# Kernel optimization log

Measured on AMD Instinct MI355X. Metric: run time of the kernel, lower is better.

The kernel has to match this reference:

```python
import jax, jax.numpy as jnp
import numpy as np
import math

N, H, E, G = 20000, 256, 320000, 1000
NF, NS = 64, 3           # sinusoid frequencies, spatial dims
DIS = 2 * NF * NS        # 384
EIN = 2 * H + 9 + DIS    # edge MLP input dim = 905


def silu(x):
    return x * jax.nn.sigmoid(x)


def sin_emb(x):
    # x: [E, 3] -> [E, 2*NF*3]
    freqs = 2.0 * math.pi * jnp.arange(NF, dtype=x.dtype)
    emb = (x[..., None] * freqs).reshape(x.shape[0], NF * NS)
    return jnp.concatenate([jnp.sin(emb), jnp.cos(emb)], axis=-1)


def layer_norm(x, gamma, beta, eps=1e-5):
    mu = jnp.mean(x, axis=-1, keepdims=True)
    var = jnp.var(x, axis=-1, keepdims=True)
    return (x - mu) * jax.lax.rsqrt(var + eps) * gamma + beta


def setup_inputs() -> dict:
    key = jax.random.key(0)
    ks = jax.random.split(key, 16)
    s = 0.02
    return {
        "node_features": jax.random.normal(ks[0], (N, H), jnp.float32),
        "lattices": jax.random.normal(ks[1], (G, 3, 3), jnp.float32),
        "edge_index": jax.random.randint(ks[2], (2, E), 0, N, dtype=jnp.int64),
        "edge2graph": jnp.sort(jax.random.randint(ks[3], (E,), 0, G, dtype=jnp.int64)),
        "frac_diff": jax.random.uniform(ks[4], (E, NS), jnp.float32),
        "num_atoms": jax.random.randint(ks[5], (G,), 0, 100, dtype=jnp.int64),
        "ln_gamma": jnp.ones((H,), jnp.float32),
        "ln_beta": jnp.zeros((H,), jnp.float32),
        "We1": jax.random.normal(ks[6], (EIN, H), jnp.float32) * s,
        "be1": jnp.zeros((H,), jnp.float32),
        "We2": jax.random.normal(ks[7], (H, H), jnp.float32) * s,
        "be2": jnp.zeros((H,), jnp.float32),
        "Wn1": jax.random.normal(ks[8], (2 * H, H), jnp.float32) * s,
        "bn1": jnp.zeros((H,), jnp.float32),
        "Wn2": jax.random.normal(ks[9], (H, H), jnp.float32) * s,
        "bn2": jnp.zeros((H,), jnp.float32),
    }


def reference(node_features, lattices, edge_index, edge2graph, frac_diff, num_atoms,
              ln_gamma, ln_beta, We1, be1, We2, be2, Wn1, bn1, Wn2, bn2):
    n = node_features.shape[0]
    h = layer_norm(node_features, ln_gamma, ln_beta)

    # edge model: gather + concat + MLP
    hi = h[edge_index[0]]                      # [E, H]
    hj = h[edge_index[1]]                      # [E, H]
    fd = sin_emb(frac_diff)                    # [E, DIS]
    ltl = jnp.einsum('gij,gkj->gik', lattices, lattices).reshape(-1, 9)  # non_symmetric: L @ L^T
    le = ltl[edge2graph]                       # [E, 9]
    x = jnp.concatenate([hi, hj, le, fd], axis=1)        # [E, EIN]
    e = silu(x @ We1 + be1)
    e = silu(e @ We2 + be2)                    # [E, H]

    # node model: scatter-mean + concat + MLP
    src = edge_index[0]
    sums = jax.ops.segment_sum(e, src, num_segments=n)   # [N, H]
    cnt = jax.ops.segment_sum(jnp.ones((e.shape[0],), e.dtype), src, num_segments=n)
    agg = sums / jnp.maximum(cnt, 1.0)[:, None]
    y = jnp.concatenate([h, agg], axis=1)                # [N, 2H]
    y = silu(y @ Wn1 + bn1)
    y = silu(y @ Wn2 + bn2)

    return node_features + y
```

## Files before the change

kernel.cpp:

```cpp
#include <hip/hip_runtime.h>

typedef unsigned short UST;
typedef __bf16 bf16x8 __attribute__((ext_vector_type(8)));
typedef float floatx4 __attribute__((ext_vector_type(4)));
typedef unsigned short ushort8v __attribute__((ext_vector_type(8)));
typedef unsigned short ushort4v __attribute__((ext_vector_type(4)));

#define N_NODES 20000
#define E_EDGES 320000
#define KE 928
#define M_PAD 20096

static __device__ __forceinline__ UST f2bf(float x){
  unsigned int u = __float_as_uint(x);
  u += 0x7fffu + ((u >> 16) & 1u);
  return (UST)(u >> 16);
}
static __device__ __forceinline__ float bf2f(UST u){
  return __uint_as_float(((unsigned int)u) << 16);
}
static __device__ __forceinline__ float siluf(float v){
  return v / (1.0f + __expf(-v));
}
static __device__ __forceinline__ void gll16(const void* g, void* lds){
  __builtin_amdgcn_global_load_lds(
      (const __attribute__((address_space(1))) unsigned int*)g,
      (__attribute__((address_space(3))) unsigned int*)lds, 16, 0, 0);
}

static __device__ __forceinline__ void mfma_step(const UST* As, const UST* Bs,
    floatx4 (&acc)[4][4], int lm, int quad, int wM, int wN){
  bf16x8 a[4], b[4];
#pragma unroll
  for (int i = 0; i < 4; ++i)
    a[i] = *(const bf16x8*)(As + (wM + i*16 + lm)*32 + quad*8);
#pragma unroll
  for (int i = 0; i < 4; ++i)
    b[i] = *(const bf16x8*)(Bs + (wN + i*16 + lm)*32 + quad*8);
#pragma unroll
  for (int mi = 0; mi < 4; ++mi)
#pragma unroll
    for (int ni = 0; ni < 4; ++ni)
      acc[mi][ni] = __builtin_amdgcn_mfma_f32_16x16x32_bf16(a[mi], b[ni], acc[mi][ni], 0, 0, 0);
}

static __device__ __forceinline__ void mfma_stage2(const UST* At, const UST* Bg,
    int Kb, floatx4 (&acc)[4][4], int lm, int quad, int wM, int wN){
#pragma unroll 2
  for (int k0 = 0; k0 < 256; k0 += 32){
    bf16x8 a[4], b[4];
#pragma unroll
    for (int i = 0; i < 4; ++i)
      a[i] = *(const bf16x8*)(At + (wM + i*16 + lm)*264 + k0 + quad*8);
#pragma unroll
    for (int i = 0; i < 4; ++i)
      b[i] = *(const bf16x8*)(Bg + (size_t)(wN + i*16 + lm)*Kb + k0 + quad*8);
#pragma unroll
    for (int mi = 0; mi < 4; ++mi)
#pragma unroll
      for (int ni = 0; ni < 4; ++ni)
        acc[mi][ni] = __builtin_amdgcn_mfma_f32_16x16x32_bf16(a[mi], b[ni], acc[mi][ni], 0, 0, 0);
  }
}

__global__ __launch_bounds__(256) void prep_all(
    const float* __restrict__ We1, const float* __restrict__ We2,
    const float* __restrict__ Wn1, const float* __restrict__ Wn2,
    const float* __restrict__ x, const float* __restrict__ gamma,
    const float* __restrict__ beta, const float* __restrict__ lat,
    const int* __restrict__ esrc, int* __restrict__ cnti,
    UST* __restrict__ W1T, UST* __restrict__ W2T,
    UST* __restrict__ Wn1T, UST* __restrict__ Wn2T,
    UST* __restrict__ h, float* __restrict__ ltl){
  int bid = blockIdx.x, t = threadIdx.x;
  if (bid < 928){
    int i = bid*256 + t;
    int n = i / KE, k = i % KE;
    float v = 0.0f;
    if (k < 512)      v = We1[(size_t)k*256 + n];
    else if (k < 896){
      int idx = k - 512, j = idx >> 1, b = idx & 1;
      v = We1[(size_t)(521 + b*192 + j)*256 + n];
    }
    else if (k < 905) v = We1[(size_t)(k-384)*256 + n];
    W1T[i] = f2bf(v);
  } else if (bid < 1184){
    int i = (bid-928)*256 + t;
    int n = i >> 8, k = i & 255;
    W2T[i]  = f2bf(We2[(size_t)k*256 + n]);
    Wn2T[i] = f2bf(Wn2[(size_t)k*256 + n]);
  } else if (bid < 1696){
    int i = (bid-1184)*256 + t;
    int n = i >> 9, k = i & 511;
    Wn1T[i] = f2bf(Wn1[(size_t)k*256 + n]);
  } else if (bid < 6696){
    int wave = t >> 6, lane = t & 63;
    int row = (bid-1696)*4 + wave;
    const float4* xp = (const float4*)(x + (size_t)row * 256);
    float4 v = xp[lane];
    float s  = v.x + v.y + v.z + v.w;
    float sq = v.x*v.x + v.y*v.y + v.z*v.z + v.w*v.w;
#pragma unroll
    for (int o = 32; o > 0; o >>= 1){ s += __shfl_xor(s, o); sq += __shfl_xor(sq, o); }
    float mu  = s * (1.0f/256.0f);
    float var = sq * (1.0f/256.0f) - mu*mu;
    float rs  = rsqrtf(var + 1e-5f);
    float4 g = ((const float4*)gamma)[lane];
    float4 b = ((const float4*)beta)[lane];
    ushort4v o4;
    o4[0] = f2bf((v.x-mu)*rs*g.x + b.x);
    o4[1] = f2bf((v.y-mu)*rs*g.y + b.y);
    o4[2] = f2bf((v.z-mu)*rs*g.z + b.z);
    o4[3] = f2bf((v.w-mu)*rs*g.w + b.w);
    *(ushort4v*)(h + (size_t)row*256 + lane*4) = o4;
  } else if (bid < 6732){
    int i = (bid-6696)*256 + t;
    if (i < 9000){
      int g = i / 9, ij = i % 9, a = ij / 3, b = ij % 3;
      const float* L = lat + g*9;
      ltl[i] = L[a*3+0]*L[b*3+0] + L[a*3+1]*L[b*3+1] + L[a*3+2]*L[b*3+2];
    }
  } else {
    int e = (bid-6732)*256 + t;
    if (e < E_EDGES) atomicAdd(&cnti[esrc[e]], 1);
  }
}

__global__ __launch_bounds__(256) void scan_kernel(const int* __restrict__ cnti,
    int* __restrict__ off, int* __restrict__ head){
  __shared__ int ps[256];
  int t = threadIdx.x;
  const int CH = 80;
  const int4* cp = (const int4*)cnti;
  int base = t * CH;
  int s = 0;
#pragma unroll 1
  for (int i = 0; i < CH/4; ++i){
    int4 v = cp[t*(CH/4) + i];
    int idx = base + i*4;
    if (idx   < N_NODES) s += v.x;
    if (idx+1 < N_NODES) s += v.y;
    if (idx+2 < N_NODES) s += v.z;
    if (idx+3 < N_NODES) s += v.w;
  }
  ps[t] = s; __syncthreads();
#pragma unroll 1
  for (int o = 1; o < 256; o <<= 1){
    int v = (t >= o) ? ps[t - o] : 0;
    __syncthreads();
    ps[t] += v;
    __syncthreads();
  }
  int run = (t > 0) ? ps[t-1] : 0;
#pragma unroll 1
  for (int i = 0; i < CH/4; ++i){
    int4 v = cp[t*(CH/4) + i];
    int idx = base + i*4;
    int a4[4] = {v.x, v.y, v.z, v.w};
#pragma unroll
    for (int j = 0; j < 4; ++j){
      int id = idx + j;
      if (id < N_NODES){ off[id] = run; head[id] = run; run += a4[j]; }
    }
  }
  if (t == 255) off[N_NODES] = run;
}

__global__ __launch_bounds__(256) void fill_kernel(const int* __restrict__ src,
    int* __restrict__ head, int* __restrict__ eidx, int* __restrict__ srcs){
  int e = blockIdx.x*256 + threadIdx.x;
  if (e < E_EDGES){
    int s = src[e];
    int p = atomicAdd(&head[s], 1);
    eidx[p] = e;
    srcs[p] = s;
  }
}

__global__ __launch_bounds__(512, 4)
void gemm_edge_fused(const UST* __restrict__ h, const int* __restrict__ ei,
                     const int* __restrict__ e2g, const float* __restrict__ fdif,
                     const float* __restrict__ ltl, const UST* __restrict__ W1T,
                     const float* __restrict__ be1, const int* __restrict__ eidx,
                     const UST* __restrict__ W2T, const float* __restrict__ be2,
                     const int* __restrict__ rownode, float* __restrict__ sums){
  __shared__ __attribute__((aligned(16))) UST lds[128*264];
  __shared__ int rn[128];
  UST* As0 = lds;
  UST* As1 = lds + 4096;
  UST* Bs0 = lds + 8192;
  UST* Bs1 = lds + 16384;
  UST* e1t = lds;
  UST* EsT = lds;
  int t = threadIdx.x;
  int bM = blockIdx.x;
  int rA = t >> 2, cA = (t & 3) * 8;
  int p0 = bM*128 + rA;
  int e0 = eidx[p0];
  int src0 = ei[e0];
  int dst0 = ei[E_EDGES + e0];
  int g0 = e2g[e0];
  float f0x = fdif[e0*3+0], f0y = fdif[e0*3+1], f0z = fdif[e0*3+2];
  size_t btb0 = (size_t)rA*KE + cA;
  size_t btb1 = btb0 + (size_t)128*KE;
  int lane = t & 63, lm = lane & 15, quad = lane >> 4;
  int wave = t >> 6, wM = (wave >> 2)*64, wN = (wave & 3)*64;
  floatx4 acc[4][4] = {};
  UST* a0d = &As0[rA*32 + cA];
  UST* a1d = &As1[rA*32 + cA];
  UST* b0d0 = &Bs0[rA*32 + cA];
  UST* b0d1 = &Bs0[(128+rA)*32 + cA];
  UST* b1d0 = &Bs1[rA*32 + cA];
  UST* b1d1 = &Bs1[(128+rA)*32 + cA];
  if (t < 128) rn[t] = rownode[bM*128 + t];

#pragma unroll 1
  for (int w = 0; w < 8; ++w){
    int k0 = w*64;
    const UST* srow = (w < 4) ? (h + (size_t)src0*256 + k0)
                              : (h + (size_t)dst0*256 + (k0 - 256));
    gll16(srow + cA,      a0d);
    gll16(srow + 32 + cA, a1d);
    gll16(W1T + btb0 + k0,      b0d0);
    gll16(W1T + btb1 + k0,      b0d1);
    gll16(W1T + btb0 + k0 + 32, b1d0);
    gll16(W1T + btb1 + k0 + 32, b1d1);
    __syncthreads();
    mfma_step(As0, Bs0, acc, lm, quad, wM, wN);
    mfma_step(As1, Bs1, acc, lm, quad, wM, wN);
    __syncthreads();
  }
#pragma unroll 1
  for (int w = 8; w < 14; ++w){
    int k0 = w*64;
    gll16(W1T + btb0 + k0,      b0d0);
    gll16(W1T + btb1 + k0,      b0d1);
    gll16(W1T + btb0 + k0 + 32, b1d0);
    gll16(W1T + btb1 + k0 + 32, b1d1);
    int jb0 = (k0 + cA - 512) >> 1;
    ushort8v o0, o1;
#pragma unroll
    for (int ii = 0; ii < 4; ++ii){
      int jj = jb0 + ii;
      int dim = jj >> 6; float kf = (float)(jj & 63);
      float fr = (dim == 0) ? f0x : ((dim == 1) ? f0y : f0z);
      float q = __builtin_amdgcn_fractf(fr * kf);
      o0[2*ii]   = f2bf(__builtin_amdgcn_sinf(q));
      o0[2*ii+1] = f2bf(__builtin_amdgcn_cosf(q));
    }
#pragma unroll
    for (int ii = 0; ii < 4; ++ii){
      int jj = jb0 + 16 + ii;
      int dim = jj >> 6; float kf = (float)(jj & 63);
      float fr = (dim == 0) ? f0x : ((dim == 1) ? f0y : f0z);
      float q = __builtin_amdgcn_fractf(fr * kf);
      o1[2*ii]   = f2bf(__builtin_amdgcn_sinf(q));
      o1[2*ii+1] = f2bf(__builtin_amdgcn_cosf(q));
    }
    *(ushort8v*)a0d = o0;
    *(ushort8v*)a1d = o1;
    __syncthreads();
    mfma_step(As0, Bs0, acc, lm, quad, wM, wN);
    mfma_step(As1, Bs1, acc, lm, quad, wM, wN);
    __syncthreads();
  }
  {
    gll16(W1T + btb0 + 896, b0d0);
    gll16(W1T + btb1 + 896, b0d1);
    ushort8v o0;
#pragma unroll
    for (int i = 0; i < 8; ++i){
      int c = cA + i;
      o0[i] = (c < 9) ? f2bf(ltl[g0*9 + c]) : (UST)0;
    }
    *(ushort8v*)a0d = o0;
    __syncthreads();
    mfma_step(As0, Bs0, acc, lm, quad, wM, wN);
  }
  __syncthreads();
#pragma unroll
  for (int mi = 0; mi < 4; ++mi)
#pragma unroll
    for (int r = 0; r < 4; ++r){
      int ml = wM + mi*16 + quad*4 + r;
#pragma unroll
      for (int ni = 0; ni < 4; ++ni){
        int nl = wN + ni*16 + lm;
        float v = acc[mi][ni][r] + be1[nl];
        e1t[ml*264 + nl] = f2bf(siluf(v));
      }
    }
  __syncthreads();

  floatx4 acc2[4][4] = {};
  mfma_stage2(e1t, W2T, 256, acc2, lm, quad, wM, wN);
  __syncthreads();

#pragma unroll
  for (int mi = 0; mi < 4; ++mi)
#pragma unroll
    for (int ni = 0; ni < 4; ++ni){
      int nl = wN + ni*16 + lm;
      int ml = wM + mi*16 + quad*4;
      ushort4v pk;
#pragma unroll
      for (int r = 0; r < 4; ++r)
        pk[r] = f2bf(siluf(acc2[mi][ni][r] + be2[nl]));
      *(ushort4v*)&EsT[nl*132 + ml] = pk;
    }
  __syncthreads();
  {
    int c = t & 255, hh = t >> 8;
    int rbeg = hh * 64;
    int cur = rn[rbeg];
    float run = 0.0f;
#pragma unroll 1
    for (int r = rbeg; r < rbeg + 64; r += 4){
      ushort4v v4 = *(const ushort4v*)&EsT[c*132 + r];
#pragma unroll
      for (int q2 = 0; q2 < 4; ++q2){
        int nd = rn[r + q2];
        if (nd != cur){ atomicAdd(&sums[(size_t)cur*256 + c], run); run = 0.0f; cur = nd; }
        run += bf2f(v4[q2]);
      }
    }
    atomicAdd(&sums[(size_t)cur*256 + c], run);
  }
}

__global__ __launch_bounds__(512, 4)
void gemm_node12(const UST* __restrict__ h, const float* __restrict__ sums,
                 const int* __restrict__ offs, const UST* __restrict__ B1,
                 const float* __restrict__ bn1, const UST* __restrict__ B2,
                 const float* __restrict__ bn2,
                 float* __restrict__ out_f, const float* __restrict__ resid){
  __shared__ __attribute__((aligned(16))) UST lds[128*264];
  UST* As0 = lds;
  UST* As1 = lds + 4096;
  UST* Bs0 = lds + 8192;
  UST* Bs1 = lds + 16384;
  UST* y1t = lds;
  int t = threadIdx.x;
  int bM = blockIdx.x;
  int rA = t >> 2, cA = (t & 3) * 8;
  int row = bM*128 + rA;
  bool valid = row < N_NODES;
  float inv = 0.0f;
  if (valid){
    int deg = offs[row+1] - offs[row];
    inv = 1.0f / fmaxf((float)deg, 1.0f);
  }
  const UST* hrow = h + (size_t)row*256;
  const float* srow = sums + (size_t)row*256;
  size_t bb0 = (size_t)rA*512 + cA;
  size_t bb1 = bb0 + (size_t)128*512;
  int lane = t & 63, lm = lane & 15, quad = lane >> 4;
  int wave = t >> 6, wM = (wave >> 2)*64, wN = (wave & 3)*64;
  floatx4 acc[4][4] = {};
  UST* a0d = &As0[rA*32 + cA];
  UST* a1d = &As1[rA*32 + cA];
  UST* b0d0 = &Bs0[rA*32 + cA];
  UST* b0d1 = &Bs0[(128+rA)*32 + cA];
  UST* b1d0 = &Bs1[rA*32 + cA];
  UST* b1d1 = &Bs1[(128+rA)*32 + cA];
  const ushort8v z8 = {0,0,0,0,0,0,0,0};
#pragma unroll 1
  for (int w = 0; w < 8; ++w){
    int k0 = w*64;
    if (k0 < 256){
      if (valid){
        gll16(hrow + k0 + cA,      a0d);
        gll16(hrow + k0 + 32 + cA, a1d);
      } else {
        *(ushort8v*)a0d = z8;
        *(ushort8v*)a1d = z8;
      }
    } else {
      ushort8v o0 = z8, o1 = z8;
      if (valid){
        int q = k0 - 256 + cA;
        float4 s0 = *(const float4*)(srow + q);
        float4 s1 = *(const float4*)(srow + q + 4);
        o0[0]=f2bf(s0.x*inv); o0[1]=f2bf(s0.y*inv); o0[2]=f2bf(s0.z*inv); o0[3]=f2bf(s0.w*inv);
        o0[4]=f2bf(s1.x*inv); o0[5]=f2bf(s1.y*inv); o0[6]=f2bf(s1.z*inv); o0[7]=f2bf(s1.w*inv);
        float4 s2 = *(const float4*)(srow + q + 32);
        float4 s3 = *(const float4*)(srow + q + 36);
        o1[0]=f2bf(s2.x*inv); o1[1]=f2bf(s2.y*inv); o1[2]=f2bf(s2.z*inv); o1[3]=f2bf(s2.w*inv);
        o1[4]=f2bf(s3.x*inv); o1[5]=f2bf(s3.y*inv); o1[6]=f2bf(s3.z*inv); o1[7]=f2bf(s3.w*inv);
      }
      *(ushort8v*)a0d = o0;
      *(ushort8v*)a1d = o1;
    }
    gll16(B1 + bb0 + k0,      b0d0);
    gll16(B1 + bb1 + k0,      b0d1);
    gll16(B1 + bb0 + k0 + 32, b1d0);
    gll16(B1 + bb1 + k0 + 32, b1d1);
    __syncthreads();
    mfma_step(As0, Bs0, acc, lm, quad, wM, wN);
    mfma_step(As1, Bs1, acc, lm, quad, wM, wN);
    __syncthreads();
  }
  __syncthreads();
#pragma unroll
  for (int mi = 0; mi < 4; ++mi)
#pragma unroll
    for (int r = 0; r < 4; ++r){
      int ml = wM + mi*16 + quad*4 + r;
#pragma unroll
      for (int ni = 0; ni < 4; ++ni){
        int nl = wN + ni*16 + lm;
        y1t[ml*264 + nl] = f2bf(siluf(acc[mi][ni][r] + bn1[nl]));
      }
    }
  __syncthreads();
  floatx4 acc2[4][4] = {};
  mfma_stage2(y1t, B2, 256, acc2, lm, quad, wM, wN);
  int mbase = bM*128 + wM + quad*4;
  int nbase = wN + lm;
#pragma unroll
  for (int mi = 0; mi < 4; ++mi)
#pragma unroll
    for (int r = 0; r < 4; ++r){
      int m = mbase + mi*16 + r;
      if (m < N_NODES){
#pragma unroll
        for (int ni = 0; ni < 4; ++ni){
          int n = nbase + ni*16;
          float v = siluf(acc2[mi][ni][r] + bn2[n]);
          out_f[(size_t)m*256 + n] = resid[(size_t)m*256 + n] + v;
        }
      }
    }
}

extern "C" void kernel_launch(void* const* d_in, const int* in_sizes, int n_in,
                              void* d_out, int out_size, void* d_ws, size_t ws_size,
                              hipStream_t stream){
  (void)in_sizes; (void)n_in; (void)out_size; (void)ws_size;
  const float* node_features = (const float*)d_in[0];
  const float* lattices      = (const float*)d_in[1];
  const int*   edge_index    = (const int*)d_in[2];
  const int*   edge2graph    = (const int*)d_in[3];
  const float* frac_diff     = (const float*)d_in[4];
  const float* ln_gamma      = (const float*)d_in[6];
  const float* ln_beta       = (const float*)d_in[7];
  const float* We1 = (const float*)d_in[8];
  const float* be1 = (const float*)d_in[9];
  const float* We2 = (const float*)d_in[10];
  const float* be2 = (const float*)d_in[11];
  const float* Wn1 = (const float*)d_in[12];
  const float* bn1 = (const float*)d_in[13];
  const float* Wn2 = (const float*)d_in[14];
  const float* bn2 = (const float*)d_in[15];

  char* w = (char*)d_ws;
  size_t off_b = 0;
  auto carve = [&](size_t bytes) -> char* {
    char* p = w + off_b; off_b += (bytes + 1023) & ~(size_t)1023; return p;
  };
  UST*   W1T  = (UST*)carve((size_t)256*KE*2);
  UST*   W2T  = (UST*)carve((size_t)256*256*2);
  UST*   Wn1T = (UST*)carve((size_t)256*512*2);
  UST*   Wn2T = (UST*)carve((size_t)256*256*2);
  UST*   hbf  = (UST*)carve((size_t)N_NODES*256*2);
  float* ltl  = (float*)carve((size_t)9000*4);
  int*   cnti = (int*)carve((size_t)20480*4);
  int*   offs = (int*)carve((size_t)(N_NODES+1)*4);
  int*   head = (int*)carve((size_t)N_NODES*4);
  int*   eidx = (int*)carve((size_t)E_EDGES*4);
  int*   srcs = (int*)carve((size_t)E_EDGES*4);
  float* sums = (float*)carve((size_t)N_NODES*256*4);

  hipMemsetAsync(cnti, 0, (size_t)20480*4, stream);
  hipMemsetAsync(sums, 0, (size_t)N_NODES*256*4, stream);

  prep_all<<<6732 + E_EDGES/256, 256, 0, stream>>>(We1, We2, Wn1, Wn2,
      node_features, ln_gamma, ln_beta, lattices, edge_index, cnti,
      W1T, W2T, Wn1T, Wn2T, hbf, ltl);

  scan_kernel<<<1, 256, 0, stream>>>(cnti, offs, head);
  fill_kernel<<<E_EDGES/256, 256, 0, stream>>>(edge_index, head, eidx, srcs);

  gemm_edge_fused<<<E_EDGES/128, 512, 0, stream>>>(
      hbf, edge_index, edge2graph, frac_diff, ltl, W1T, be1, eidx,
      W2T, be2, srcs, sums);

  gemm_node12<<<M_PAD/128, 512, 0, stream>>>(
      hbf, sums, offs, Wn1T, bn1, Wn2T, bn2, (float*)d_out, node_features);
}
```

Before: 495.2 us.

## Load MFMA operands directly from global memory instead of LDS staging

Both fused GEMM kernels drop the LDS double-buffer staging (global_load_lds plus two barriers per K step). Each lane now loads its bf16x8 A and B fragments straight from global memory into registers, and the sinusoidal and lattice features are computed directly in registers. This removes the barriers and LDS traffic, but each wave now fetches its own copies of the W1 and node rows. That lowers data reuse, adds redundant sin/cos work across waves, and leaves global-load latency less hidden.

```diff
diff --git a/kernel.cpp b/kernel.cpp
--- a/kernel.cpp
+++ b/kernel.cpp
@@ -21,27 +21,6 @@
 }
 static __device__ __forceinline__ float siluf(float v){
   return v / (1.0f + __expf(-v));
-}
-static __device__ __forceinline__ void gll16(const void* g, void* lds){
-  __builtin_amdgcn_global_load_lds(
-      (const __attribute__((address_space(1))) unsigned int*)g,
-      (__attribute__((address_space(3))) unsigned int*)lds, 16, 0, 0);
-}
-
-static __device__ __forceinline__ void mfma_step(const UST* As, const UST* Bs,
-    floatx4 (&acc)[4][4], int lm, int quad, int wM, int wN){
-  bf16x8 a[4], b[4];
-#pragma unroll
-  for (int i = 0; i < 4; ++i)
-    a[i] = *(const bf16x8*)(As + (wM + i*16 + lm)*32 + quad*8);
-#pragma unroll
-  for (int i = 0; i < 4; ++i)
-    b[i] = *(const bf16x8*)(Bs + (wN + i*16 + lm)*32 + quad*8);
-#pragma unroll
-  for (int mi = 0; mi < 4; ++mi)
-#pragma unroll
-    for (int ni = 0; ni < 4; ++ni)
-      acc[mi][ni] = __builtin_amdgcn_mfma_f32_16x16x32_bf16(a[mi], b[ni], acc[mi][ni], 0, 0, 0);
 }
 
 static __device__ __forceinline__ void mfma_stage2(const UST* At, const UST* Bg,
@@ -186,98 +165,108 @@
                      const int* __restrict__ rownode, float* __restrict__ sums){
   __shared__ __attribute__((aligned(16))) UST lds[128*264];
   __shared__ int rn[128];
-  UST* As0 = lds;
-  UST* As1 = lds + 4096;
-  UST* Bs0 = lds + 8192;
-  UST* Bs1 = lds + 16384;
   UST* e1t = lds;
   UST* EsT = lds;
   int t = threadIdx.x;
   int bM = blockIdx.x;
-  int rA = t >> 2, cA = (t & 3) * 8;
-  int p0 = bM*128 + rA;
-  int e0 = eidx[p0];
-  int src0 = ei[e0];
-  int dst0 = ei[E_EDGES + e0];
-  int g0 = e2g[e0];
-  float f0x = fdif[e0*3+0], f0y = fdif[e0*3+1], f0z = fdif[e0*3+2];
-  size_t btb0 = (size_t)rA*KE + cA;
-  size_t btb1 = btb0 + (size_t)128*KE;
   int lane = t & 63, lm = lane & 15, quad = lane >> 4;
   int wave = t >> 6, wM = (wave >> 2)*64, wN = (wave & 3)*64;
+  if (t < 128) rn[t] = rownode[bM*128 + t];
+
+  int eR[4], aoff[4], boff[4];
+#pragma unroll
+  for (int i = 0; i < 4; ++i){
+    eR[i]   = eidx[bM*128 + wM + i*16 + lm];
+    aoff[i] = ei[eR[i]] * 256;
+    boff[i] = (wN + i*16 + lm) * KE;
+  }
   floatx4 acc[4][4] = {};
-  UST* a0d = &As0[rA*32 + cA];
-  UST* a1d = &As1[rA*32 + cA];
-  UST* b0d0 = &Bs0[rA*32 + cA];
-  UST* b0d1 = &Bs0[(128+rA)*32 + cA];
-  UST* b1d0 = &Bs1[rA*32 + cA];
-  UST* b1d1 = &Bs1[(128+rA)*32 + cA];
-  if (t < 128) rn[t] = rownode[bM*128 + t];
-
-#pragma unroll 1
-  for (int w = 0; w < 8; ++w){
-    int k0 = w*64;
-    const UST* srow = (w < 4) ? (h + (size_t)src0*256 + k0)
-                              : (h + (size_t)dst0*256 + (k0 - 256));
-    gll16(srow + cA,      a0d);
-    gll16(srow + 32 + cA, a1d);
-    gll16(W1T + btb0 + k0,      b0d0);
-    gll16(W1T + btb1 + k0,      b0d1);
-    gll16(W1T + btb0 + k0 + 32, b1d0);
-    gll16(W1T + btb1 + k0 + 32, b1d1);
-    __syncthreads();
-    mfma_step(As0, Bs0, acc, lm, quad, wM, wN);
-    mfma_step(As1, Bs1, acc, lm, quad, wM, wN);
-    __syncthreads();
-  }
-#pragma unroll 1
-  for (int w = 8; w < 14; ++w){
-    int k0 = w*64;
-    gll16(W1T + btb0 + k0,      b0d0);
-    gll16(W1T + btb1 + k0,      b0d1);
-    gll16(W1T + btb0 + k0 + 32, b1d0);
-    gll16(W1T + btb1 + k0 + 32, b1d1);
-    int jb0 = (k0 + cA - 512) >> 1;
-    ushort8v o0, o1;
-#pragma unroll
-    for (int ii = 0; ii < 4; ++ii){
-      int jj = jb0 + ii;
-      int dim = jj >> 6; float kf = (float)(jj & 63);
-      float fr = (dim == 0) ? f0x : ((dim == 1) ? f0y : f0z);
-      float q = __builtin_amdgcn_fractf(fr * kf);
-      o0[2*ii]   = f2bf(__builtin_amdgcn_sinf(q));
-      o0[2*ii+1] = f2bf(__builtin_amdgcn_cosf(q));
-    }
-#pragma unroll
-    for (int ii = 0; ii < 4; ++ii){
-      int jj = jb0 + 16 + ii;
-      int dim = jj >> 6; float kf = (float)(jj & 63);
-      float fr = (dim == 0) ? f0x : ((dim == 1) ? f0y : f0z);
-      float q = __builtin_amdgcn_fractf(fr * kf);
-      o1[2*ii]   = f2bf(__builtin_amdgcn_sinf(q));
-      o1[2*ii+1] = f2bf(__builtin_amdgcn_cosf(q));
-    }
-    *(ushort8v*)a0d = o0;
-    *(ushort8v*)a1d = o1;
-    __syncthreads();
-    mfma_step(As0, Bs0, acc, lm, quad, wM, wN);
-    mfma_step(As1, Bs1, acc, lm, quad, wM, wN);
-    __syncthreads();
+
+#pragma unroll 2
+  for (int c = 0; c < 8; ++c){
+    int k = c*32 + quad*8;
+    bf16x8 a[4], b[4];
+#pragma unroll
+    for (int i = 0; i < 4; ++i) a[i] = *(const bf16x8*)(h + aoff[i] + k);
+#pragma unroll
+    for (int i = 0; i < 4; ++i) b[i] = *(const bf16x8*)(W1T + boff[i] + c*32 + quad*8);
+#pragma unroll
+    for (int mi = 0; mi < 4; ++mi)
+#pragma unroll
+      for (int ni = 0; ni < 4; ++ni)
+        acc[mi][ni] = __builtin_amdgcn_mfma_f32_16x16x32_bf16(a[mi], b[ni], acc[mi][ni], 0, 0, 0);
+  }
+#pragma unroll
+  for (int i = 0; i < 4; ++i) aoff[i] = ei[E_EDGES + eR[i]] * 256;
+#pragma unroll 2
+  for (int c = 8; c < 16; ++c){
+    int k = (c-8)*32 + quad*8;
+    bf16x8 a[4], b[4];
+#pragma unroll
+    for (int i = 0; i < 4; ++i) a[i] = *(const bf16x8*)(h + aoff[i] + k);
+#pragma unroll
+    for (int i = 0; i < 4; ++i) b[i] = *(const bf16x8*)(W1T + boff[i] + c*32 + quad*8);
+#pragma unroll
+    for (int mi = 0; mi < 4; ++mi)
+#pragma unroll
+      for (int ni = 0; ni < 4; ++ni)
+        acc[mi][ni] = __builtin_amdgcn_mfma_f32_16x16x32_bf16(a[mi], b[ni], acc[mi][ni], 0, 0, 0);
+  }
+  float fr[4][3];
+#pragma unroll
+  for (int i = 0; i < 4; ++i){
+    fr[i][0] = fdif[eR[i]*3 + 0];
+    fr[i][1] = fdif[eR[i]*3 + 1];
+    fr[i][2] = fdif[eR[i]*3 + 2];
+  }
+#pragma unroll 1
+  for (int c = 16; c < 28; ++c){
+    int jb = (c-16)*16 + quad*4;
+    ushort8v av[4];
+#pragma unroll
+    for (int p = 0; p < 4; ++p){
+      int jj = jb + p;
+      int dim = jj >> 6;
+      float kf = (float)(jj & 63);
+#pragma unroll
+      for (int i = 0; i < 4; ++i){
+        float f = (dim == 0) ? fr[i][0] : ((dim == 1) ? fr[i][1] : fr[i][2]);
+        float q = __builtin_amdgcn_fractf(f * kf);
+        av[i][2*p]   = f2bf(__builtin_amdgcn_sinf(q));
+        av[i][2*p+1] = f2bf(__builtin_amdgcn_cosf(q));
+      }
+    }
+    bf16x8 b[4];
+#pragma unroll
+    for (int i = 0; i < 4; ++i) b[i] = *(const bf16x8*)(W1T + boff[i] + c*32 + quad*8);
+#pragma unroll
+    for (int mi = 0; mi < 4; ++mi)
+#pragma unroll
+      for (int ni = 0; ni < 4; ++ni)
+        acc[mi][ni] = __builtin_amdgcn_mfma_f32_16x16x32_bf16(
+            *(const bf16x8*)&av[mi], b[ni], acc[mi][ni], 0, 0, 0);
   }
   {
-    gll16(W1T + btb0 + 896, b0d0);
-    gll16(W1T + btb1 + 896, b0d1);
-    ushort8v o0;
-#pragma unroll
-    for (int i = 0; i < 8; ++i){
-      int c = cA + i;
-      o0[i] = (c < 9) ? f2bf(ltl[g0*9 + c]) : (UST)0;
-    }
-    *(ushort8v*)a0d = o0;
-    __syncthreads();
-    mfma_step(As0, Bs0, acc, lm, quad, wM, wN);
-  }
-  __syncthreads();
+    ushort8v av[4];
+#pragma unroll
+    for (int i = 0; i < 4; ++i){
+      int gg = e2g[eR[i]] * 9;
+#pragma unroll
+      for (int j = 0; j < 8; ++j){
+        int c9 = quad*8 + j;
+        av[i][j] = (c9 < 9) ? f2bf(ltl[gg + c9]) : (UST)0;
+      }
+    }
+    bf16x8 b[4];
+#pragma unroll
+    for (int i = 0; i < 4; ++i) b[i] = *(const bf16x8*)(W1T + boff[i] + 896 + quad*8);
+#pragma unroll
+    for (int mi = 0; mi < 4; ++mi)
+#pragma unroll
+      for (int ni = 0; ni < 4; ++ni)
+        acc[mi][ni] = __builtin_amdgcn_mfma_f32_16x16x32_bf16(
+            *(const bf16x8*)&av[mi], b[ni], acc[mi][ni], 0, 0, 0);
+  }
 #pragma unroll
   for (int mi = 0; mi < 4; ++mi)
 #pragma unroll
@@ -335,72 +324,64 @@
                  const float* __restrict__ bn2,
                  float* __restrict__ out_f, const float* __restrict__ resid){
   __shared__ __attribute__((aligned(16))) UST lds[128*264];
-  UST* As0 = lds;
-  UST* As1 = lds + 4096;
-  UST* Bs0 = lds + 8192;
-  UST* Bs1 = lds + 16384;
   UST* y1t = lds;
   int t = threadIdx.x;
   int bM = blockIdx.x;
-  int rA = t >> 2, cA = (t & 3) * 8;
-  int row = bM*128 + rA;
-  bool valid = row < N_NODES;
-  float inv = 0.0f;
-  if (valid){
-    int deg = offs[row+1] - offs[row];
-    inv = 1.0f / fmaxf((float)deg, 1.0f);
-  }
-  const UST* hrow = h + (size_t)row*256;
-  const float* srow = sums + (size_t)row*256;
-  size_t bb0 = (size_t)rA*512 + cA;
-  size_t bb1 = bb0 + (size_t)128*512;
   int lane = t & 63, lm = lane & 15, quad = lane >> 4;
   int wave = t >> 6, wM = (wave >> 2)*64, wN = (wave & 3)*64;
+  int rowg[4]; bool val[4]; float inv[4]; int boff[4];
+#pragma unroll
+  for (int i = 0; i < 4; ++i){
+    rowg[i] = bM*128 + wM + i*16 + lm;
+    val[i] = rowg[i] < N_NODES;
+    int deg = val[i] ? (offs[rowg[i]+1] - offs[rowg[i]]) : 1;
+    inv[i] = 1.0f / fmaxf((float)deg, 1.0f);
+    boff[i] = (wN + i*16 + lm) * 512;
+  }
+  const ushort8v z8 = {0,0,0,0,0,0,0,0};
   floatx4 acc[4][4] = {};
-  UST* a0d = &As0[rA*32 + cA];
-  UST* a1d = &As1[rA*32 + cA];
-  UST* b0d0 = &Bs0[rA*32 + cA];
-  UST* b0d1 = &Bs0[(128+rA)*32 + cA];
-  UST* b1d0 = &Bs1[rA*32 + cA];
-  UST* b1d1 = &Bs1[(128+rA)*32 + cA];
-  const ushort8v z8 = {0,0,0,0,0,0,0,0};
-#pragma unroll 1
-  for (int w = 0; w < 8; ++w){
-    int k0 = w*64;
-    if (k0 < 256){
-      if (valid){
-        gll16(hrow + k0 + cA,      a0d);
-        gll16(hrow + k0 + 32 + cA, a1d);
-      } else {
-        *(ushort8v*)a0d = z8;
-        *(ushort8v*)a1d = z8;
-      }
-    } else {
-      ushort8v o0 = z8, o1 = z8;
-      if (valid){
-        int q = k0 - 256 + cA;
-        float4 s0 = *(const float4*)(srow + q);
-        float4 s1 = *(const float4*)(srow + q + 4);
-        o0[0]=f2bf(s0.x*inv); o0[1]=f2bf(s0.y*inv); o0[2]=f2bf(s0.z*inv); o0[3]=f2bf(s0.w*inv);
-        o0[4]=f2bf(s1.x*inv); o0[5]=f2bf(s1.y*inv); o0[6]=f2bf(s1.z*inv); o0[7]=f2bf(s1.w*inv);
-        float4 s2 = *(const float4*)(srow + q + 32);
-        float4 s3 = *(const float4*)(srow + q + 36);
-        o1[0]=f2bf(s2.x*inv); o1[1]=f2bf(s2.y*inv); o1[2]=f2bf(s2.z*inv); o1[3]=f2bf(s2.w*inv);
-        o1[4]=f2bf(s3.x*inv); o1[5]=f2bf(s3.y*inv); o1[6]=f2bf(s3.z*inv); o1[7]=f2bf(s3.w*inv);
-      }
-      *(ushort8v*)a0d = o0;
-      *(ushort8v*)a1d = o1;
-    }
-    gll16(B1 + bb0 + k0,      b0d0);
-    gll16(B1 + bb1 + k0,      b0d1);
-    gll16(B1 + bb0 + k0 + 32, b1d0);
-    gll16(B1 + bb1 + k0 + 32, b1d1);
-    __syncthreads();
-    mfma_step(As0, Bs0, acc, lm, quad, wM, wN);
-    mfma_step(As1, Bs1, acc, lm, quad, wM, wN);
-    __syncthreads();
-  }
-  __syncthreads();
+#pragma unroll 2
+  for (int c = 0; c < 8; ++c){
+    int k = c*32 + quad*8;
+    bf16x8 a[4], b[4];
+#pragma unroll
+    for (int i = 0; i < 4; ++i)
+      a[i] = val[i] ? *(const bf16x8*)(h + (size_t)rowg[i]*256 + k) : *(const bf16x8*)&z8;
+#pragma unroll
+    for (int i = 0; i < 4; ++i) b[i] = *(const bf16x8*)(B1 + boff[i] + c*32 + quad*8);
+#pragma unroll
+    for (int mi = 0; mi < 4; ++mi)
+#pragma unroll
+      for (int ni = 0; ni < 4; ++ni)
+        acc[mi][ni] = __builtin_amdgcn_mfma_f32_16x16x32_bf16(a[mi], b[ni], acc[mi][ni], 0, 0, 0);
+  }
+#pragma unroll 1
+  for (int c = 8; c < 16; ++c){
+    int k = (c-8)*32 + quad*8;
+    ushort8v av[4];
+#pragma unroll
+    for (int i = 0; i < 4; ++i){
+      av[i] = z8;
+      if (val[i]){
+        const float* sp = sums + (size_t)rowg[i]*256 + k;
+        float4 s0 = *(const float4*)sp;
+        float4 s1 = *(const float4*)(sp + 4);
+        av[i][0]=f2bf(s0.x*inv[i]); av[i][1]=f2bf(s0.y*inv[i]);
+        av[i][2]=f2bf(s0.z*inv[i]); av[i][3]=f2bf(s0.w*inv[i]);
+        av[i][4]=f2bf(s1.x*inv[i]); av[i][5]=f2bf(s1.y*inv[i]);
+        av[i][6]=f2bf(s1.z*inv[i]); av[i][7]=f2bf(s1.w*inv[i]);
+      }
+    }
+    bf16x8 b[4];
+#pragma unroll
+    for (int i = 0; i < 4; ++i) b[i] = *(const bf16x8*)(B1 + boff[i] + c*32 + quad*8);
+#pragma unroll
+    for (int mi = 0; mi < 4; ++mi)
+#pragma unroll
+      for (int ni = 0; ni < 4; ++ni)
+        acc[mi][ni] = __builtin_amdgcn_mfma_f32_16x16x32_bf16(
+            *(const bf16x8*)&av[mi], b[ni], acc[mi][ni], 0, 0, 0);
+  }
 #pragma unroll
   for (int mi = 0; mi < 4; ++mi)
 #pragma unroll
```

New measurement: 697.8 us. 1.41x slower.
